# Performance work log

Hardware: AMD Instinct MI355X
Metric: run time of the kernel (lower is better)

The kernel has to match this reference:

```python
import jax, jax.numpy as jnp
import numpy as np

B, D, E, H = 8192, 2048, 8, 128

def setup_inputs() -> dict:
    key = jax.random.key(0)
    ks = jax.random.split(key, 9)
    s_d = 1.0 / np.sqrt(D)
    s_h = 1.0 / np.sqrt(H)
    return {
        "x": jax.random.normal(ks[0], (B, D), dtype=jnp.float32),
        "gate_w": jax.random.normal(ks[1], (D, E), dtype=jnp.float32) * s_d,
        "gate_b": jnp.zeros((E,), dtype=jnp.float32),
        "W1": jax.random.normal(ks[2], (E, D, H), dtype=jnp.float32) * s_d,
        "b1": jnp.zeros((E, H), dtype=jnp.float32),
        "W2": jax.random.normal(ks[3], (E, H, H), dtype=jnp.float32) * s_h,
        "b2": jnp.zeros((E, H), dtype=jnp.float32),
        "W3": jax.random.normal(ks[4], (E, H, D), dtype=jnp.float32) * s_h,
        "b3": jnp.zeros((E, D), dtype=jnp.float32),
    }

def reference(x, gate_w, gate_b, W1, b1, W2, b2, W3, b3):
    # Adaptive gate: softmax over experts
    gates = jax.nn.softmax(x @ gate_w + gate_b, axis=1)          # [B, E]
    # All experts as one batched (grouped) GEMM over the expert axis.
    h1 = jax.nn.silu(jnp.einsum('bd,edh->ebh', x, W1) + b1[:, None, :])   # [E, B, H]
    h2 = jax.nn.silu(jnp.einsum('ebh,ehk->ebk', h1, W2) + b2[:, None, :]) # [E, B, H]
    y = jnp.einsum('ebh,ehd->ebd', h2, W3) + b3[:, None, :]               # [E, B, D]
    # Gate-weighted sum over experts (fused reduction, no [B,E,D] stack kept)
    out = jnp.einsum('be,ebd->bd', gates, y)                     # [B, D]
    return out
```

## Files before the change

kernel.cpp:

```cpp
#include <hip/hip_runtime.h>


typedef __attribute__((ext_vector_type(8))) short short8;
typedef __attribute__((ext_vector_type(4))) float f32x4;

#define B_SZ 8192
#define D_SZ 2048
#define E_SZ 8
#define H_SZ 128

__device__ __forceinline__ short f2bf(float f) {
  unsigned u = __builtin_bit_cast(unsigned, f);
  unsigned r = (u + 0x7fffu + ((u >> 16) & 1u)) >> 16;
  return (short)r;
}

__device__ __forceinline__ float bf2f(short s) {
  return __builtin_bit_cast(float, (unsigned)((unsigned short)s) << 16);
}

__device__ __forceinline__ float silu_f(float v) {
  return v / (1.f + __expf(-v));
}

__device__ __forceinline__ void gload_lds16(const void* g, void* l) {
  __builtin_amdgcn_global_load_lds(
      (const __attribute__((address_space(1))) void*)g,
      (__attribute__((address_space(3))) void*)l,
      16, 0, 0);
}

template<int NHT>
__device__ __forceinline__ void core128(const short* __restrict__ A,
                                        const short* __restrict__ B,
                                        short* lds, f32x4 acc[4][4])
{
  const int tid  = threadIdx.x;
  const int lane = tid & 63;
  const int wid  = tid >> 6;
  const int wr = wid >> 1, wc = wid & 1;
  const int lm = lane & 15, lk = lane >> 4;
  const int wl = (tid & ~63) * 8;

  auto STAGE = [&](int eta) {
    const size_t go = (size_t)(eta >> 1)*8192 + (size_t)(eta & 1)*4096;
    short* l = lds + (eta & 1)*8192;
    gload_lds16(A + go + tid*8,        l + wl);
    gload_lds16(A + go + 2048 + tid*8, l + 2048 + wl);
    gload_lds16(B + go + tid*8,        l + 4096 + wl);
    gload_lds16(B + go + 2048 + tid*8, l + 6144 + wl);
  };

  STAGE(0);
  __syncthreads();
  for (int eta = 0; eta < NHT; ++eta) {
    if (eta + 1 < NHT) STAGE(eta + 1);
    const short* la = lds + (eta & 1)*8192 + lk*1024 + (wr*64 + lm)*8;
    const short* lb = lds + (eta & 1)*8192 + 4096 + lk*1024 + (wc*64 + lm)*8;
    short8 av[4], bv[4];
    #pragma unroll
    for (int f = 0; f < 4; ++f) av[f] = *(const short8*)(la + f*128);
    #pragma unroll
    for (int f = 0; f < 4; ++f) bv[f] = *(const short8*)(lb + f*128);
    #pragma unroll
    for (int i = 0; i < 4; ++i)
      #pragma unroll
      for (int j = 0; j < 4; ++j)
        acc[i][j] = __builtin_amdgcn_mfma_f32_16x16x32_bf16(av[i], bv[j], acc[i][j], 0, 0, 0);
    __syncthreads();
  }
}

__global__ __launch_bounds__(256)
void k_convert(const float* __restrict__ x,  const float* __restrict__ W1,
               const float* __restrict__ W2, const float* __restrict__ W3,
               short* __restrict__ xf, short* __restrict__ w1f,
               short* __restrict__ w2f, short* __restrict__ w3f)
{
  const int gi = blockIdx.x * 256 + threadIdx.x;
  if (gi < 2097152) {
    const int t = gi >> 10, r = gi & 1023;
    const int bt = t >> 5, kt = t & 31;
    const int kg = r >> 7, p = r & 127;
    const float* src = x + (size_t)(bt*128 + p)*2048 + kt*64 + kg*8;
    const float4 v0 = *(const float4*)src;
    const float4 v1 = *(const float4*)(src + 4);
    short8 o;
    o[0]=f2bf(v0.x); o[1]=f2bf(v0.y); o[2]=f2bf(v0.z); o[3]=f2bf(v0.w);
    o[4]=f2bf(v1.x); o[5]=f2bf(v1.y); o[6]=f2bf(v1.z); o[7]=f2bf(v1.w);
    *(short8*)(xf + (size_t)gi*8) = o;
  } else if (gi < 2097152 + 262144) {
    const int g = gi - 2097152;
    const int t = g >> 10, r = g & 1023;
    const int e = t >> 5, kt = t & 31;
    const int kg = r >> 7, p = r & 127;
    const int k0 = kt*64 + kg*8;
    short8 o;
    #pragma unroll
    for (int j = 0; j < 8; ++j)
      o[j] = f2bf(W1[(size_t)e*262144 + (size_t)(k0 + j)*128 + p]);
    *(short8*)(w1f + (size_t)g*8) = o;
  } else if (gi < 2097152 + 262144 + 16384) {
    const int g = gi - (2097152 + 262144);
    const int t = g >> 10, r = g & 1023;
    const int e = t >> 1, kt = t & 1;
    const int kg = r >> 7, p = r & 127;
    const int k0 = kt*64 + kg*8;
    short8 o;
    #pragma unroll
    for (int j = 0; j < 8; ++j)
      o[j] = f2bf(W2[(size_t)e*16384 + (size_t)(k0 + j)*128 + p]);
    *(short8*)(w2f + (size_t)g*8) = o;
  } else if (gi < 2637824) {
    const int g = gi - 2375680;
    const int t = g >> 10, r = g & 1023;
    const int nt = t >> 4, kt = t & 15;
    const int kg = r >> 7, p = r & 127;
    const int k0 = kt*64 + kg*8;
    short8 o;
    #pragma unroll
    for (int j = 0; j < 8; ++j) {
      const int k = k0 + j;
      o[j] = f2bf(W3[(size_t)(k >> 7)*262144 + (size_t)(k & 127)*2048 + nt*128 + p]);
    }
    *(short8*)(w3f + (size_t)g*8) = o;
  }
}

__global__ __launch_bounds__(256)
void k_gate(const float* __restrict__ x, const float* __restrict__ gw,
            const float* __restrict__ gb, float* __restrict__ gates)
{
  const int wid = threadIdx.x >> 6, lane = threadIdx.x & 63;
  const int row = blockIdx.x * 4 + wid;
  const float* xr = x + (size_t)row * 2048;
  float acc[8] = {0.f,0.f,0.f,0.f,0.f,0.f,0.f,0.f};
  for (int it = 0; it < 32; ++it) {
    const int k = it*64 + lane;
    const float xv = xr[k];
    const float4 g0 = *(const float4*)(gw + (size_t)k*8);
    const float4 g1 = *(const float4*)(gw + (size_t)k*8 + 4);
    acc[0] += xv*g0.x; acc[1] += xv*g0.y; acc[2] += xv*g0.z; acc[3] += xv*g0.w;
    acc[4] += xv*g1.x; acc[5] += xv*g1.y; acc[6] += xv*g1.z; acc[7] += xv*g1.w;
  }
  #pragma unroll
  for (int e = 0; e < 8; ++e) {
    #pragma unroll
    for (int d = 1; d < 64; d <<= 1)
      acc[e] += __shfl_xor(acc[e], d, 64);
  }
  if (lane == 0) {
    float lg[8], mx = -1e30f;
    #pragma unroll
    for (int e = 0; e < 8; ++e) { lg[e] = acc[e] + gb[e]; mx = fmaxf(mx, lg[e]); }
    float s = 0.f;
    #pragma unroll
    for (int e = 0; e < 8; ++e) { lg[e] = __expf(lg[e] - mx); s += lg[e]; }
    const float inv = 1.f / s;
    #pragma unroll
    for (int e = 0; e < 8; ++e) gates[(size_t)row*8 + e] = lg[e] * inv;
  }
}

__global__ __launch_bounds__(256, 4)
void k_gemm1s(const short* __restrict__ xf, const short* __restrict__ w1f,
              short* __restrict__ p)
{
  __shared__ short lds[16384];
  const int b = blockIdx.x;
  const int xcd = b & 7, idx = b >> 3;
  const int bt = xcd*8 + (idx & 7);
  const int rest = idx >> 3;
  const int nt = rest & 7, kh = rest >> 3;

  f32x4 acc[4][4] = {};
  core128<32>(xf  + ((size_t)bt*32 + kh*16)*8192,
              w1f + ((size_t)nt*32 + kh*16)*8192,
              lds, acc);

  const int tid = threadIdx.x, lane = tid & 63, wid = tid >> 6;
  const int wr = wid >> 1, wc = wid & 1, lm = lane & 15, lr = lane >> 4;
  short* pd = p + (size_t)kh*8388608;
  #pragma unroll
  for (int fm = 0; fm < 4; ++fm)
  #pragma unroll
  for (int i = 0; i < 4; ++i) {
    const int m = bt*128 + wr*64 + fm*16 + lr*4 + i;
    #pragma unroll
    for (int fn = 0; fn < 4; ++fn) {
      const int n = nt*128 + wc*64 + fn*16 + lm;
      pd[(size_t)m*1024 + n] = f2bf(acc[fm][fn][i]);
    }
  }
}

__global__ __launch_bounds__(256, 2)
void k_gemm2m(const short* __restrict__ p, const short* __restrict__ w2f,
              const float* __restrict__ b1, const float* __restrict__ b2,
              const float* __restrict__ gates, short* __restrict__ h2gf)
{
  __shared__ short lds[32768];
  const int bt2 = blockIdx.x, e = blockIdx.y;
  const int tid = threadIdx.x;
  const int wlds = (tid & ~63) * 8;

  #pragma unroll
  for (int q = 0; q < 8; ++q)
    gload_lds16(w2f + (size_t)e*16384 + q*2048 + tid*8,
                lds + 16384 + q*2048 + wlds);

  #pragma unroll
  for (int u = 0; u < 8; ++u) {
    const int g = u*256 + tid;
    const int m = g >> 4, hg = g & 15;
    const size_t src = (size_t)(bt2*128 + m)*1024 + e*128 + hg*8;
    const short8 a = *(const short8*)(p + src);
    const short8 c = *(const short8*)(p + 8388608 + src);
    short8 o;
    #pragma unroll
    for (int j = 0; j < 8; ++j) {
      const float v = bf2f(a[j]) + bf2f(c[j]) + b1[e*128 + hg*8 + j];
      o[j] = f2bf(silu_f(v));
    }
    *(short8*)(lds + (hg>>3)*8192 + (hg&7)*1024 + m*8) = o;
  }
  asm volatile("s_waitcnt vmcnt(0)" ::: "memory");
  __syncthreads();

  const int lane = tid & 63, wid = tid >> 6;
  const int wr = wid >> 1, wc = wid & 1, lm = lane & 15, lk = lane >> 4, lr = lane >> 4;
  f32x4 acc[4][4] = {};
  #pragma unroll
  for (int kt = 0; kt < 2; ++kt)
  #pragma unroll
  for (int ks = 0; ks < 2; ++ks) {
    short8 av[4], bv[4];
    #pragma unroll
    for (int f = 0; f < 4; ++f)
      av[f] = *(const short8*)(lds + kt*8192 + (ks*4+lk)*1024 + (wr*64 + f*16 + lm)*8);
    #pragma unroll
    for (int f = 0; f < 4; ++f)
      bv[f] = *(const short8*)(lds + 16384 + kt*8192 + (ks*4+lk)*1024 + (wc*64 + f*16 + lm)*8);
    #pragma unroll
    for (int i = 0; i < 4; ++i)
      #pragma unroll
      for (int j = 0; j < 4; ++j)
        acc[i][j] = __builtin_amdgcn_mfma_f32_16x16x32_bf16(av[i], bv[j], acc[i][j], 0, 0, 0);
  }
  __syncthreads();

  #pragma unroll
  for (int fm = 0; fm < 4; ++fm)
  #pragma unroll
  for (int i = 0; i < 4; ++i) {
    const int m = wr*64 + fm*16 + lr*4 + i;
    const float g = gates[(size_t)(bt2*128 + m)*8 + e];
    #pragma unroll
    for (int fn = 0; fn < 4; ++fn) {
      const int h = wc*64 + fn*16 + lm;
      const float v = silu_f(acc[fm][fn][i] + b2[e*128 + h]) * g;
      lds[(h>>6)*8192 + ((h>>3)&7)*1024 + m*8 + (h&7)] = f2bf(v);
    }
  }
  __syncthreads();

  #pragma unroll
  for (int q = 0; q < 8; ++q) {
    const int g = q*256 + tid;
    const int li = g*8;
    const int t2 = li >> 13, o = li & 8191;
    *(short8*)(h2gf + ((size_t)bt2*16 + e*2 + t2)*8192 + o) = *(const short8*)(lds + li);
  }
}

__global__ __launch_bounds__(256, 4)
void k_gemm3(const short* __restrict__ h2gf, const short* __restrict__ w3f,
             const float* __restrict__ b3, const float* __restrict__ gates,
             float* __restrict__ out)
{
  __shared__ short lds[16384];
  const int b = blockIdx.x;
  const int xcd = b & 7, idx = b >> 3;
  const int bt = xcd*8 + (idx & 7);
  const int nt = idx >> 3;

  f32x4 acc[4][4] = {};
  core128<32>(h2gf + (size_t)bt*16*8192,
              w3f  + (size_t)nt*16*8192,
              lds, acc);

  const int tid = threadIdx.x, lane = tid & 63, wid = tid >> 6;
  const int wr = wid >> 1, wc = wid & 1, lm = lane & 15, lr = lane >> 4;
  float b3c[4][8];
  #pragma unroll
  for (int fn = 0; fn < 4; ++fn) {
    const int n = nt*128 + wc*64 + fn*16 + lm;
    #pragma unroll
    for (int e = 0; e < 8; ++e) b3c[fn][e] = b3[(size_t)e*D_SZ + n];
  }
  #pragma unroll
  for (int fm = 0; fm < 4; ++fm)
  #pragma unroll
  for (int i = 0; i < 4; ++i) {
    const int m = bt*128 + wr*64 + fm*16 + lr*4 + i;
    const float4 ga  = *(const float4*)(gates + (size_t)m*8);
    const float4 gbv = *(const float4*)(gates + (size_t)m*8 + 4);
    #pragma unroll
    for (int fn = 0; fn < 4; ++fn) {
      const int n = nt*128 + wc*64 + fn*16 + lm;
      const float bias = ga.x*b3c[fn][0] + ga.y*b3c[fn][1] + ga.z*b3c[fn][2] + ga.w*b3c[fn][3]
                       + gbv.x*b3c[fn][4] + gbv.y*b3c[fn][5] + gbv.z*b3c[fn][6] + gbv.w*b3c[fn][7];
      out[(size_t)m*D_SZ + n] = acc[fm][fn][i] + bias;
    }
  }
}

extern "C" void kernel_launch(void* const* d_in, const int* in_sizes, int n_in,
                              void* d_out, int out_size, void* d_ws, size_t ws_size,
                              hipStream_t stream)
{
  (void)in_sizes; (void)n_in; (void)out_size; (void)ws_size;
  const float* x  = (const float*)d_in[0];
  const float* gw = (const float*)d_in[1];
  const float* gb = (const float*)d_in[2];
  const float* W1 = (const float*)d_in[3];
  const float* b1 = (const float*)d_in[4];
  const float* W2 = (const float*)d_in[5];
  const float* b2 = (const float*)d_in[6];
  const float* W3 = (const float*)d_in[7];
  const float* b3 = (const float*)d_in[8];
  float* out = (float*)d_out;

  char* ws = (char*)d_ws;
  short* xf    = (short*)ws;  ws += (size_t)B_SZ*D_SZ*2;
  short* w1f   = (short*)ws;  ws += (size_t)E_SZ*D_SZ*H_SZ*2;
  short* w2f   = (short*)ws;  ws += (size_t)E_SZ*H_SZ*H_SZ*2;
  short* w3f   = (short*)ws;  ws += (size_t)E_SZ*H_SZ*D_SZ*2;
  float* gates = (float*)ws;  ws += (size_t)B_SZ*E_SZ*4;
  short* p     = (short*)ws;  ws += (size_t)2*B_SZ*1024*2;
  short* h2gf  = (short*)ws;  ws += (size_t)B_SZ*E_SZ*H_SZ*2;

  k_convert<<<dim3(10304), dim3(256), 0, stream>>>(x, W1, W2, W3, xf, w1f, w2f, w3f);
  k_gate   <<<dim3(2048),  dim3(256), 0, stream>>>(x, gw, gb, gates);
  k_gemm1s <<<dim3(1024),  dim3(256), 0, stream>>>(xf, w1f, p);
  k_gemm2m <<<dim3(64, 8), dim3(256), 0, stream>>>(p, w2f, b1, b2, gates, h2gf);
  k_gemm3  <<<dim3(1024),  dim3(256), 0, stream>>>(h2gf, w3f, b3, gates, out);
}
```

Baseline: 156.8 us.

## Halve gemm2 row tile, load W2 fragments to registers, swizzle LDS

Measured after the change: 156.0 us. Within noise of the previous version (-0.5%).

```diff
diff --git a/kernel.cpp b/kernel.cpp
--- a/kernel.cpp
+++ b/kernel.cpp
@@ -194,82 +194,91 @@
   }
 }
 
-__global__ __launch_bounds__(256, 2)
+__global__ __launch_bounds__(256, 4)
 void k_gemm2m(const short* __restrict__ p, const short* __restrict__ w2f,
               const float* __restrict__ b1, const float* __restrict__ b2,
               const float* __restrict__ gates, short* __restrict__ h2gf)
 {
-  __shared__ short lds[32768];
+  __shared__ short lds[8192];
   const int bt2 = blockIdx.x, e = blockIdx.y;
   const int tid = threadIdx.x;
-  const int wlds = (tid & ~63) * 8;
-
-  #pragma unroll
-  for (int q = 0; q < 8; ++q)
-    gload_lds16(w2f + (size_t)e*16384 + q*2048 + tid*8,
-                lds + 16384 + q*2048 + wlds);
-
-  #pragma unroll
-  for (int u = 0; u < 8; ++u) {
-    const int g = u*256 + tid;
-    const int m = g >> 4, hg = g & 15;
-    const size_t src = (size_t)(bt2*128 + m)*1024 + e*128 + hg*8;
+  const int lane = tid & 63, wid = tid >> 6;
+  const int wr = wid >> 1, wc = wid & 1;
+  const int lm = lane & 15, lk = lane >> 4, lr = lane >> 4;
+
+  short8 bvAll[2][2][4];
+  #pragma unroll
+  for (int kt = 0; kt < 2; ++kt)
+  #pragma unroll
+  for (int ks = 0; ks < 2; ++ks)
+  #pragma unroll
+  for (int fn = 0; fn < 4; ++fn)
+    bvAll[kt][ks][fn] = *(const short8*)(
+        w2f + (size_t)e*16384 + kt*8192 + (ks*4 + lk)*1024
+            + (wc*64 + fn*16 + lm)*8);
+
+  const int hg = tid & 15;
+  const int mb = tid >> 4;
+  const float4 b1a = *(const float4*)(b1 + e*128 + hg*8);
+  const float4 b1b = *(const float4*)(b1 + e*128 + hg*8 + 4);
+  const float b1r[8] = {b1a.x, b1a.y, b1a.z, b1a.w, b1b.x, b1b.y, b1b.z, b1b.w};
+  #pragma unroll
+  for (int u = 0; u < 4; ++u) {
+    const int m = u*16 + mb;
+    const size_t src = (size_t)(bt2*64 + m)*1024 + e*128 + hg*8;
     const short8 a = *(const short8*)(p + src);
     const short8 c = *(const short8*)(p + 8388608 + src);
     short8 o;
     #pragma unroll
     for (int j = 0; j < 8; ++j) {
-      const float v = bf2f(a[j]) + bf2f(c[j]) + b1[e*128 + hg*8 + j];
+      const float v = bf2f(a[j]) + bf2f(c[j]) + b1r[j];
       o[j] = f2bf(silu_f(v));
     }
-    *(short8*)(lds + (hg>>3)*8192 + (hg&7)*1024 + m*8) = o;
-  }
-  asm volatile("s_waitcnt vmcnt(0)" ::: "memory");
+    *(short8*)(lds + hg*512 + (m ^ (hg & 7))*8) = o;
+  }
   __syncthreads();
 
-  const int lane = tid & 63, wid = tid >> 6;
-  const int wr = wid >> 1, wc = wid & 1, lm = lane & 15, lk = lane >> 4, lr = lane >> 4;
-  f32x4 acc[4][4] = {};
+  f32x4 acc[2][4] = {};
   #pragma unroll
   for (int kt = 0; kt < 2; ++kt)
   #pragma unroll
   for (int ks = 0; ks < 2; ++ks) {
-    short8 av[4], bv[4];
-    #pragma unroll
-    for (int f = 0; f < 4; ++f)
-      av[f] = *(const short8*)(lds + kt*8192 + (ks*4+lk)*1024 + (wr*64 + f*16 + lm)*8);
-    #pragma unroll
-    for (int f = 0; f < 4; ++f)
-      bv[f] = *(const short8*)(lds + 16384 + kt*8192 + (ks*4+lk)*1024 + (wc*64 + f*16 + lm)*8);
-    #pragma unroll
-    for (int i = 0; i < 4; ++i)
+    const int kg = kt*8 + ks*4 + lk;
+    short8 av[2];
+    #pragma unroll
+    for (int f = 0; f < 2; ++f)
+      av[f] = *(const short8*)(lds + kg*512 + ((wr*32 + f*16 + lm) ^ (kg & 7))*8);
+    #pragma unroll
+    for (int fm = 0; fm < 2; ++fm)
       #pragma unroll
-      for (int j = 0; j < 4; ++j)
-        acc[i][j] = __builtin_amdgcn_mfma_f32_16x16x32_bf16(av[i], bv[j], acc[i][j], 0, 0, 0);
+      for (int fn = 0; fn < 4; ++fn)
+        acc[fm][fn] = __builtin_amdgcn_mfma_f32_16x16x32_bf16(
+            av[fm], bvAll[kt][ks][fn], acc[fm][fn], 0, 0, 0);
   }
   __syncthreads();
 
   #pragma unroll
-  for (int fm = 0; fm < 4; ++fm)
+  for (int fm = 0; fm < 2; ++fm)
   #pragma unroll
   for (int i = 0; i < 4; ++i) {
-    const int m = wr*64 + fm*16 + lr*4 + i;
-    const float g = gates[(size_t)(bt2*128 + m)*8 + e];
+    const int m = wr*32 + fm*16 + lr*4 + i;
+    const float g = gates[(size_t)(bt2*64 + m)*8 + e];
     #pragma unroll
     for (int fn = 0; fn < 4; ++fn) {
       const int h = wc*64 + fn*16 + lm;
       const float v = silu_f(acc[fm][fn][i] + b2[e*128 + h]) * g;
-      lds[(h>>6)*8192 + ((h>>3)&7)*1024 + m*8 + (h&7)] = f2bf(v);
+      lds[wc*4096 + (fn*2 + (lm >> 3))*512 + m*8 + (lm & 7)] = f2bf(v);
     }
   }
   __syncthreads();
 
   #pragma unroll
-  for (int q = 0; q < 8; ++q) {
-    const int g = q*256 + tid;
-    const int li = g*8;
-    const int t2 = li >> 13, o = li & 8191;
-    *(short8*)(h2gf + ((size_t)bt2*16 + e*2 + t2)*8192 + o) = *(const short8*)(lds + li);
+  for (int q = 0; q < 4; ++q) {
+    const int li = q*2048 + tid*8;
+    const int t2 = li >> 12, kg = (li >> 9) & 7, rem = li & 511;
+    short* dst = h2gf + ((size_t)(bt2 >> 1)*16 + e*2 + t2)*8192
+               + kg*1024 + (bt2 & 1)*512 + rem;
+    *(short8*)dst = *(const short8*)(lds + li);
   }
 }
 
@@ -343,6 +352,6 @@
   k_convert<<<dim3(10304), dim3(256), 0, stream>>>(x, W1, W2, W3, xf, w1f, w2f, w3f);
   k_gate   <<<dim3(2048),  dim3(256), 0, stream>>>(x, gw, gb, gates);
   k_gemm1s <<<dim3(1024),  dim3(256), 0, stream>>>(xf, w1f, p);
-  k_gemm2m <<<dim3(64, 8), dim3(256), 0, stream>>>(p, w2f, b1, b2, gates, h2gf);
+  k_gemm2m <<<dim3(128, 8), dim3(256), 0, stream>>>(p, w2f, b1, b2, gates, h2gf);
   k_gemm3  <<<dim3(1024),  dim3(256), 0, stream>>>(h2gf, w3f, b3, gates, out);
 }
```

## Fuse GEMM1 with GEMM2 per expert tile and merge convert with gate

Applied to the files above, without the earlier changes.

New measurement: 147.2 us. 1.07x faster.

```diff
diff --git a/kernel.cpp b/kernel.cpp
--- a/kernel.cpp
+++ b/kernel.cpp
@@ -13,10 +13,6 @@
   unsigned u = __builtin_bit_cast(unsigned, f);
   unsigned r = (u + 0x7fffu + ((u >> 16) & 1u)) >> 16;
   return (short)r;
-}
-
-__device__ __forceinline__ float bf2f(short s) {
-  return __builtin_bit_cast(float, (unsigned)((unsigned short)s) << 16);
 }
 
 __device__ __forceinline__ float silu_f(float v) {
@@ -72,204 +68,193 @@
 }
 
 __global__ __launch_bounds__(256)
-void k_convert(const float* __restrict__ x,  const float* __restrict__ W1,
-               const float* __restrict__ W2, const float* __restrict__ W3,
-               short* __restrict__ xf, short* __restrict__ w1f,
-               short* __restrict__ w2f, short* __restrict__ w3f)
-{
-  const int gi = blockIdx.x * 256 + threadIdx.x;
-  if (gi < 2097152) {
-    const int t = gi >> 10, r = gi & 1023;
-    const int bt = t >> 5, kt = t & 31;
-    const int kg = r >> 7, p = r & 127;
-    const float* src = x + (size_t)(bt*128 + p)*2048 + kt*64 + kg*8;
-    const float4 v0 = *(const float4*)src;
-    const float4 v1 = *(const float4*)(src + 4);
-    short8 o;
-    o[0]=f2bf(v0.x); o[1]=f2bf(v0.y); o[2]=f2bf(v0.z); o[3]=f2bf(v0.w);
-    o[4]=f2bf(v1.x); o[5]=f2bf(v1.y); o[6]=f2bf(v1.z); o[7]=f2bf(v1.w);
-    *(short8*)(xf + (size_t)gi*8) = o;
-  } else if (gi < 2097152 + 262144) {
-    const int g = gi - 2097152;
-    const int t = g >> 10, r = g & 1023;
-    const int e = t >> 5, kt = t & 31;
-    const int kg = r >> 7, p = r & 127;
-    const int k0 = kt*64 + kg*8;
-    short8 o;
-    #pragma unroll
-    for (int j = 0; j < 8; ++j)
-      o[j] = f2bf(W1[(size_t)e*262144 + (size_t)(k0 + j)*128 + p]);
-    *(short8*)(w1f + (size_t)g*8) = o;
-  } else if (gi < 2097152 + 262144 + 16384) {
-    const int g = gi - (2097152 + 262144);
-    const int t = g >> 10, r = g & 1023;
-    const int e = t >> 1, kt = t & 1;
-    const int kg = r >> 7, p = r & 127;
-    const int k0 = kt*64 + kg*8;
-    short8 o;
-    #pragma unroll
-    for (int j = 0; j < 8; ++j)
-      o[j] = f2bf(W2[(size_t)e*16384 + (size_t)(k0 + j)*128 + p]);
-    *(short8*)(w2f + (size_t)g*8) = o;
-  } else if (gi < 2637824) {
-    const int g = gi - 2375680;
-    const int t = g >> 10, r = g & 1023;
-    const int nt = t >> 4, kt = t & 15;
-    const int kg = r >> 7, p = r & 127;
-    const int k0 = kt*64 + kg*8;
-    short8 o;
-    #pragma unroll
-    for (int j = 0; j < 8; ++j) {
-      const int k = k0 + j;
-      o[j] = f2bf(W3[(size_t)(k >> 7)*262144 + (size_t)(k & 127)*2048 + nt*128 + p]);
-    }
-    *(short8*)(w3f + (size_t)g*8) = o;
-  }
-}
-
-__global__ __launch_bounds__(256)
-void k_gate(const float* __restrict__ x, const float* __restrict__ gw,
-            const float* __restrict__ gb, float* __restrict__ gates)
-{
-  const int wid = threadIdx.x >> 6, lane = threadIdx.x & 63;
-  const int row = blockIdx.x * 4 + wid;
-  const float* xr = x + (size_t)row * 2048;
-  float acc[8] = {0.f,0.f,0.f,0.f,0.f,0.f,0.f,0.f};
-  for (int it = 0; it < 32; ++it) {
-    const int k = it*64 + lane;
-    const float xv = xr[k];
-    const float4 g0 = *(const float4*)(gw + (size_t)k*8);
-    const float4 g1 = *(const float4*)(gw + (size_t)k*8 + 4);
-    acc[0] += xv*g0.x; acc[1] += xv*g0.y; acc[2] += xv*g0.z; acc[3] += xv*g0.w;
-    acc[4] += xv*g1.x; acc[5] += xv*g1.y; acc[6] += xv*g1.z; acc[7] += xv*g1.w;
-  }
-  #pragma unroll
-  for (int e = 0; e < 8; ++e) {
-    #pragma unroll
-    for (int d = 1; d < 64; d <<= 1)
-      acc[e] += __shfl_xor(acc[e], d, 64);
-  }
-  if (lane == 0) {
-    float lg[8], mx = -1e30f;
-    #pragma unroll
-    for (int e = 0; e < 8; ++e) { lg[e] = acc[e] + gb[e]; mx = fmaxf(mx, lg[e]); }
-    float s = 0.f;
-    #pragma unroll
-    for (int e = 0; e < 8; ++e) { lg[e] = __expf(lg[e] - mx); s += lg[e]; }
-    const float inv = 1.f / s;
-    #pragma unroll
-    for (int e = 0; e < 8; ++e) gates[(size_t)row*8 + e] = lg[e] * inv;
-  }
-}
-
-__global__ __launch_bounds__(256, 4)
-void k_gemm1s(const short* __restrict__ xf, const short* __restrict__ w1f,
-              short* __restrict__ p)
+void k_cvt_gate(const float* __restrict__ x,  const float* __restrict__ W1,
+                const float* __restrict__ W2, const float* __restrict__ W3,
+                const float* __restrict__ gw, const float* __restrict__ gb,
+                short* __restrict__ xf, short* __restrict__ w1f,
+                short* __restrict__ w2f, short* __restrict__ w3f,
+                float* __restrict__ gates)
+{
+  if (blockIdx.x < 10304) {
+    const int gi = blockIdx.x * 256 + threadIdx.x;
+    if (gi < 2097152) {
+      const int t = gi >> 10, r = gi & 1023;
+      const int bt = t >> 5, kt = t & 31;
+      const int kg = r >> 7, p = r & 127;
+      const float* src = x + (size_t)(bt*128 + p)*2048 + kt*64 + kg*8;
+      const float4 v0 = *(const float4*)src;
+      const float4 v1 = *(const float4*)(src + 4);
+      short8 o;
+      o[0]=f2bf(v0.x); o[1]=f2bf(v0.y); o[2]=f2bf(v0.z); o[3]=f2bf(v0.w);
+      o[4]=f2bf(v1.x); o[5]=f2bf(v1.y); o[6]=f2bf(v1.z); o[7]=f2bf(v1.w);
+      *(short8*)(xf + (size_t)gi*8) = o;
+    } else if (gi < 2097152 + 262144) {
+      const int g = gi - 2097152;
+      const int t = g >> 10, r = g & 1023;
+      const int e = t >> 5, kt = t & 31;
+      const int kg = r >> 7, p = r & 127;
+      const int k0 = kt*64 + kg*8;
+      short8 o;
+      #pragma unroll
+      for (int j = 0; j < 8; ++j)
+        o[j] = f2bf(W1[(size_t)e*262144 + (size_t)(k0 + j)*128 + p]);
+      *(short8*)(w1f + (size_t)g*8) = o;
+    } else if (gi < 2097152 + 262144 + 16384) {
+      const int g = gi - (2097152 + 262144);
+      const int t = g >> 10, r = g & 1023;
+      const int e = t >> 1, kt = t & 1;
+      const int kg = r >> 7, p = r & 127;
+      const int k0 = kt*64 + kg*8;
+      short8 o;
+      #pragma unroll
+      for (int j = 0; j < 8; ++j)
+        o[j] = f2bf(W2[(size_t)e*16384 + (size_t)(k0 + j)*128 + p]);
+      *(short8*)(w2f + (size_t)g*8) = o;
+    } else if (gi < 2637824) {
+      const int g = gi - 2375680;
+      const int t = g >> 10, r = g & 1023;
+      const int nt = t >> 4, kt = t & 15;
+      const int kg = r >> 7, p = r & 127;
+      const int k0 = kt*64 + kg*8;
+      short8 o;
+      #pragma unroll
+      for (int j = 0; j < 8; ++j) {
+        const int k = k0 + j;
+        o[j] = f2bf(W3[(size_t)(k >> 7)*262144 + (size_t)(k & 127)*2048 + nt*128 + p]);
+      }
+      *(short8*)(w3f + (size_t)g*8) = o;
+    }
+  } else {
+    const int wid = threadIdx.x >> 6, lane = threadIdx.x & 63;
+    const int row = (blockIdx.x - 10304) * 4 + wid;
+    const float* xr = x + (size_t)row * 2048;
+    float acc[8] = {0.f,0.f,0.f,0.f,0.f,0.f,0.f,0.f};
+    for (int it = 0; it < 32; ++it) {
+      const int k = it*64 + lane;
+      const float xv = xr[k];
+      const float4 g0 = *(const float4*)(gw + (size_t)k*8);
+      const float4 g1 = *(const float4*)(gw + (size_t)k*8 + 4);
+      acc[0] += xv*g0.x; acc[1] += xv*g0.y; acc[2] += xv*g0.z; acc[3] += xv*g0.w;
+      acc[4] += xv*g1.x; acc[5] += xv*g1.y; acc[6] += xv*g1.z; acc[7] += xv*g1.w;
+    }
+    #pragma unroll
+    for (int e = 0; e < 8; ++e) {
+      #pragma unroll
+      for (int d = 1; d < 64; d <<= 1)
+        acc[e] += __shfl_xor(acc[e], d, 64);
+    }
+    if (lane == 0) {
+      float lg[8], mx = -1e30f;
+      #pragma unroll
+      for (int e = 0; e < 8; ++e) { lg[e] = acc[e] + gb[e]; mx = fmaxf(mx, lg[e]); }
+      float s = 0.f;
+      #pragma unroll
+      for (int e = 0; e < 8; ++e) { lg[e] = __expf(lg[e] - mx); s += lg[e]; }
+      const float inv = 1.f / s;
+      #pragma unroll
+      for (int e = 0; e < 8; ++e) gates[(size_t)row*8 + e] = lg[e] * inv;
+    }
+  }
+}
+
+__global__ __launch_bounds__(256, 2)
+void k_gemm12f(const short* __restrict__ xf, const short* __restrict__ w1f,
+               const short* __restrict__ w2f,
+               const float* __restrict__ b1, const float* __restrict__ b2,
+               const float* __restrict__ gates, short* __restrict__ h2gf)
 {
   __shared__ short lds[16384];
   const int b = blockIdx.x;
   const int xcd = b & 7, idx = b >> 3;
   const int bt = xcd*8 + (idx & 7);
-  const int rest = idx >> 3;
-  const int nt = rest & 7, kh = rest >> 3;
+  const int e  = idx >> 3;
 
   f32x4 acc[4][4] = {};
-  core128<32>(xf  + ((size_t)bt*32 + kh*16)*8192,
-              w1f + ((size_t)nt*32 + kh*16)*8192,
+  core128<64>(xf  + (size_t)bt*32*8192,
+              w1f + (size_t)e*32*8192,
               lds, acc);
 
   const int tid = threadIdx.x, lane = tid & 63, wid = tid >> 6;
-  const int wr = wid >> 1, wc = wid & 1, lm = lane & 15, lr = lane >> 4;
-  short* pd = p + (size_t)kh*8388608;
+  const int wr = wid >> 1, wc = wid & 1;
+  const int lm = lane & 15, lk = lane >> 4, lr = lane >> 4;
+
+  short8 bvAll[2][2][4];
+  #pragma unroll
+  for (int kt = 0; kt < 2; ++kt)
+  #pragma unroll
+  for (int ks = 0; ks < 2; ++ks)
+  #pragma unroll
+  for (int fn = 0; fn < 4; ++fn)
+    bvAll[kt][ks][fn] = *(const short8*)(
+        w2f + (size_t)e*16384 + kt*8192 + (ks*4 + lk)*1024
+            + (wc*64 + fn*16 + lm)*8);
+
+  float gv[4][4];
   #pragma unroll
   for (int fm = 0; fm < 4; ++fm)
   #pragma unroll
-  for (int i = 0; i < 4; ++i) {
-    const int m = bt*128 + wr*64 + fm*16 + lr*4 + i;
-    #pragma unroll
-    for (int fn = 0; fn < 4; ++fn) {
-      const int n = nt*128 + wc*64 + fn*16 + lm;
-      pd[(size_t)m*1024 + n] = f2bf(acc[fm][fn][i]);
-    }
-  }
-}
-
-__global__ __launch_bounds__(256, 2)
-void k_gemm2m(const short* __restrict__ p, const short* __restrict__ w2f,
-              const float* __restrict__ b1, const float* __restrict__ b2,
-              const float* __restrict__ gates, short* __restrict__ h2gf)
-{
-  __shared__ short lds[32768];
-  const int bt2 = blockIdx.x, e = blockIdx.y;
-  const int tid = threadIdx.x;
-  const int wlds = (tid & ~63) * 8;
-
-  #pragma unroll
-  for (int q = 0; q < 8; ++q)
-    gload_lds16(w2f + (size_t)e*16384 + q*2048 + tid*8,
-                lds + 16384 + q*2048 + wlds);
-
-  #pragma unroll
-  for (int u = 0; u < 8; ++u) {
-    const int g = u*256 + tid;
-    const int m = g >> 4, hg = g & 15;
-    const size_t src = (size_t)(bt2*128 + m)*1024 + e*128 + hg*8;
-    const short8 a = *(const short8*)(p + src);
-    const short8 c = *(const short8*)(p + 8388608 + src);
-    short8 o;
-    #pragma unroll
-    for (int j = 0; j < 8; ++j) {
-      const float v = bf2f(a[j]) + bf2f(c[j]) + b1[e*128 + hg*8 + j];
-      o[j] = f2bf(silu_f(v));
-    }
-    *(short8*)(lds + (hg>>3)*8192 + (hg&7)*1024 + m*8) = o;
-  }
-  asm volatile("s_waitcnt vmcnt(0)" ::: "memory");
-  __syncthreads();
-
-  const int lane = tid & 63, wid = tid >> 6;
-  const int wr = wid >> 1, wc = wid & 1, lm = lane & 15, lk = lane >> 4, lr = lane >> 4;
-  f32x4 acc[4][4] = {};
-  #pragma unroll
-  for (int kt = 0; kt < 2; ++kt)
-  #pragma unroll
-  for (int ks = 0; ks < 2; ++ks) {
-    short8 av[4], bv[4];
-    #pragma unroll
-    for (int f = 0; f < 4; ++f)
-      av[f] = *(const short8*)(lds + kt*8192 + (ks*4+lk)*1024 + (wr*64 + f*16 + lm)*8);
-    #pragma unroll
-    for (int f = 0; f < 4; ++f)
-      bv[f] = *(const short8*)(lds + 16384 + kt*8192 + (ks*4+lk)*1024 + (wc*64 + f*16 + lm)*8);
-    #pragma unroll
-    for (int i = 0; i < 4; ++i)
-      #pragma unroll
-      for (int j = 0; j < 4; ++j)
-        acc[i][j] = __builtin_amdgcn_mfma_f32_16x16x32_bf16(av[i], bv[j], acc[i][j], 0, 0, 0);
-  }
-  __syncthreads();
-
+  for (int i = 0; i < 4; ++i)
+    gv[fm][i] = gates[(size_t)(bt*128 + wr*64 + fm*16 + lr*4 + i)*8 + e];
+
+  float b1v[4];
+  #pragma unroll
+  for (int fn = 0; fn < 4; ++fn) b1v[fn] = b1[e*H_SZ + wc*64 + fn*16 + lm];
   #pragma unroll
   for (int fm = 0; fm < 4; ++fm)
   #pragma unroll
   for (int i = 0; i < 4; ++i) {
     const int m = wr*64 + fm*16 + lr*4 + i;
-    const float g = gates[(size_t)(bt2*128 + m)*8 + e];
     #pragma unroll
     for (int fn = 0; fn < 4; ++fn) {
-      const int h = wc*64 + fn*16 + lm;
-      const float v = silu_f(acc[fm][fn][i] + b2[e*128 + h]) * g;
-      lds[(h>>6)*8192 + ((h>>3)&7)*1024 + m*8 + (h&7)] = f2bf(v);
+      const int n = wc*64 + fn*16 + lm;
+      const float v = silu_f(acc[fm][fn][i] + b1v[fn]);
+      lds[(n >> 3)*1024 + m*8 + (n & 7)] = f2bf(v);
     }
   }
   __syncthreads();
 
+  f32x4 acc2[4][4] = {};
+  #pragma unroll
+  for (int kt = 0; kt < 2; ++kt)
+  #pragma unroll
+  for (int ks = 0; ks < 2; ++ks) {
+    short8 av[4];
+    #pragma unroll
+    for (int f = 0; f < 4; ++f)
+      av[f] = *(const short8*)(lds + (kt*8 + ks*4 + lk)*1024 + (wr*64 + f*16 + lm)*8);
+    #pragma unroll
+    for (int i = 0; i < 4; ++i)
+      #pragma unroll
+      for (int j = 0; j < 4; ++j)
+        acc2[i][j] = __builtin_amdgcn_mfma_f32_16x16x32_bf16(
+            av[i], bvAll[kt][ks][j], acc2[i][j], 0, 0, 0);
+  }
+  __syncthreads();
+
+  float b2v[4];
+  #pragma unroll
+  for (int fn = 0; fn < 4; ++fn) b2v[fn] = b2[e*H_SZ + wc*64 + fn*16 + lm];
+  #pragma unroll
+  for (int fm = 0; fm < 4; ++fm)
+  #pragma unroll
+  for (int i = 0; i < 4; ++i) {
+    const int m = wr*64 + fm*16 + lr*4 + i;
+    const float g = gv[fm][i];
+    #pragma unroll
+    for (int fn = 0; fn < 4; ++fn) {
+      const int n = wc*64 + fn*16 + lm;
+      const float v = silu_f(acc2[fm][fn][i] + b2v[fn]) * g;
+      lds[(n >> 3)*1024 + m*8 + (n & 7)] = f2bf(v);
+    }
+  }
+  __syncthreads();
+
   #pragma unroll
   for (int q = 0; q < 8; ++q) {
-    const int g = q*256 + tid;
-    const int li = g*8;
-    const int t2 = li >> 13, o = li & 8191;
-    *(short8*)(h2gf + ((size_t)bt2*16 + e*2 + t2)*8192 + o) = *(const short8*)(lds + li);
+    const int li = q*2048 + tid*8;
+    const int t2 = li >> 13, off = li & 8191;
+    *(short8*)(h2gf + ((size_t)bt*16 + e*2 + t2)*8192 + off) =
+        *(const short8*)(lds + li);
   }
 }
 
@@ -337,12 +322,10 @@
   short* w2f   = (short*)ws;  ws += (size_t)E_SZ*H_SZ*H_SZ*2;
   short* w3f   = (short*)ws;  ws += (size_t)E_SZ*H_SZ*D_SZ*2;
   float* gates = (float*)ws;  ws += (size_t)B_SZ*E_SZ*4;
-  short* p     = (short*)ws;  ws += (size_t)2*B_SZ*1024*2;
   short* h2gf  = (short*)ws;  ws += (size_t)B_SZ*E_SZ*H_SZ*2;
 
-  k_convert<<<dim3(10304), dim3(256), 0, stream>>>(x, W1, W2, W3, xf, w1f, w2f, w3f);
-  k_gate   <<<dim3(2048),  dim3(256), 0, stream>>>(x, gw, gb, gates);
-  k_gemm1s <<<dim3(1024),  dim3(256), 0, stream>>>(xf, w1f, p);
-  k_gemm2m <<<dim3(64, 8), dim3(256), 0, stream>>>(p, w2f, b1, b2, gates, h2gf);
-  k_gemm3  <<<dim3(1024),  dim3(256), 0, stream>>>(h2gf, w3f, b3, gates, out);
-}
+  k_cvt_gate<<<dim3(12352), dim3(256), 0, stream>>>(x, W1, W2, W3, gw, gb,
+                                                    xf, w1f, w2f, w3f, gates);
+  k_gemm12f <<<dim3(512),  dim3(256), 0, stream>>>(xf, w1f, w2f, b1, b2, gates, h2gf);
+  k_gemm3   <<<dim3(1024), dim3(256), 0, stream>>>(h2gf, w3f, b3, gates, out);
+}
```
